# Performance work log

Measured on AMD Instinct MI355X. Metric: run time of the kernel, lower is better.

Reference implementation:

```python
import jax, jax.numpy as jnp
import numpy as np

N = 100000        # nodes
E = 3200000       # edges (avg degree 32)
B = 64            # graphs in the batch
IN_DIM = 128
HEADS = 4
C1 = 8            # conv1 out_channels per head
C2 = 4            # conv2 out_channels per head
OUT_DIM = 10
EPS = 1e-16       # PyG softmax denominator eps


def _lin(key, fan_in, fan_out):
    return jax.random.normal(key, (fan_in, fan_out), jnp.float32) / np.sqrt(fan_in)


def setup_inputs() -> dict:
    key = jax.random.key(0)
    ks = jax.random.split(key, 16)
    x = jax.random.normal(ks[0], (N, IN_DIM), jnp.float32)
    edge_index = jax.random.randint(ks[1], (2, E), 0, N)
    batch = jnp.sort(jax.random.randint(ks[2], (N,), 0, B))
    d1 = HEADS * C1  # 32
    d2 = HEADS * C2  # 16
    inp = {
        "x": x, "edge_index": edge_index, "batch": batch,
        # conv1 (TransformerConv in=128 -> heads*8 = 32)
        "Wq1": _lin(ks[3], IN_DIM, d1), "bq1": jnp.zeros((d1,), jnp.float32),
        "Wk1": _lin(ks[4], IN_DIM, d1), "bk1": jnp.zeros((d1,), jnp.float32),
        "Wv1": _lin(ks[5], IN_DIM, d1), "bv1": jnp.zeros((d1,), jnp.float32),
        "Ws1": _lin(ks[6], IN_DIM, d1), "bs1": jnp.zeros((d1,), jnp.float32),
        # conv2 (in=32 -> heads*4 = 16)
        "Wq2": _lin(ks[7], d1, d2), "bq2": jnp.zeros((d2,), jnp.float32),
        "Wk2": _lin(ks[8], d1, d2), "bk2": jnp.zeros((d2,), jnp.float32),
        "Wv2": _lin(ks[9], d1, d2), "bv2": jnp.zeros((d2,), jnp.float32),
        "Ws2": _lin(ks[10], d1, d2), "bs2": jnp.zeros((d2,), jnp.float32),
        # fc (16 -> 10)
        "Wfc": _lin(ks[11], d2, OUT_DIM), "bfc": jnp.zeros((OUT_DIM,), jnp.float32),
    }
    return inp


def transformer_conv(x, src, dst, Wq, bq, Wk, bk, Wv, bv, Ws, bs, heads):
    n = x.shape[0]
    hc = Wq.shape[1]
    c = hc // heads
    q = (x @ Wq + bq).reshape(n, heads, c)
    k = (x @ Wk + bk).reshape(n, heads, c)
    v = (x @ Wv + bv).reshape(n, heads, c)
    # edge-wise attention logits: query at dst, key at src -> [E, H]
    alpha = jnp.einsum('ehc,ehc->eh', q[dst], k[src]) / np.sqrt(c).astype(np.float32)
    # segment softmax over incoming edges of each dst node
    amax = jax.ops.segment_max(alpha, dst, num_segments=n)           # [N,H]
    ea = jnp.exp(alpha - amax[dst])
    denom = jax.ops.segment_sum(ea, dst, num_segments=n)             # [N,H]
    w = ea / (denom[dst] + EPS)                                      # [E,H]
    msg = v[src] * w[:, :, None]                                     # [E,H,C]
    out = jax.ops.segment_sum(msg, dst, num_segments=n).reshape(n, hc)
    return out + x @ Ws + bs  # root/skip connection


def reference(x, edge_index, batch,
              Wq1, bq1, Wk1, bk1, Wv1, bv1, Ws1, bs1,
              Wq2, bq2, Wk2, bk2, Wv2, bv2, Ws2, bs2,
              Wfc, bfc):
    src, dst = edge_index[0], edge_index[1]
    h = transformer_conv(x, src, dst, Wq1, bq1, Wk1, bk1, Wv1, bv1, Ws1, bs1, HEADS)
    h = jax.nn.relu(h)
    h = transformer_conv(h, src, dst, Wq2, bq2, Wk2, bk2, Wv2, bv2, Ws2, bs2, HEADS)
    h = jax.nn.relu(h)
    # global mean pool per graph
    sums = jax.ops.segment_sum(h, batch, num_segments=B)             # [B,16]
    cnt = jax.ops.segment_sum(jnp.ones((h.shape[0],), h.dtype), batch, num_segments=B)
    pooled = sums / jnp.maximum(cnt, 1.0)[:, None]
    return pooled @ Wfc + bfc                                        # [B,OUT_DIM]
```

## Files before the change

kernel.cpp:

```cpp
#include <hip/hip_runtime.h>

#define HEADS 4
#define EPS 1e-16f
#define NR 256
#define EPB 2048

typedef float floatx2 __attribute__((ext_vector_type(2)));
typedef short bf16x8 __attribute__((ext_vector_type(8)));
typedef float f32x4 __attribute__((ext_vector_type(4)));

__device__ inline unsigned short f2bf(float f) {
    union { float f; unsigned u; } v; v.f = f;
    unsigned r = v.u + 0x7FFFu + ((v.u >> 16) & 1u);
    return (unsigned short)(r >> 16);
}
__device__ inline unsigned char f2fp8(float f) {
    return (unsigned char)(__builtin_amdgcn_cvt_pk_fp8_f32(f, 0.f, 0u, false) & 0xFF);
}

__device__ inline int rangeOf(int dst, int rdiv, float rinv) {
    int q = (int)((float)dst * rinv);
    if (q > NR - 1) q = NR - 1;
    if ((long long)q * rdiv > dst) --q;
    else if ((long long)(q + 1) * rdiv <= dst) ++q;
    return q;
}

__global__ __launch_bounds__(256) void scatter_count(
    const int* __restrict__ ei, int E, int rdiv, float rinv,
    int* __restrict__ pcnt)
{
    __shared__ int cnt[NR];
    int b = blockIdx.x, t = threadIdx.x;
    int b0 = b * EPB;
    int nloc = min(EPB, E - b0);
    cnt[t] = 0;
    __syncthreads();
    #pragma unroll
    for (int u = 0; u < 8; ++u) {
        int li = u * 256 + t;
        if (li < nloc)
            atomicAdd(&cnt[rangeOf(ei[E + b0 + li], rdiv, rinv)], 1);
    }
    __syncthreads();
    pcnt[(size_t)b * NR + t] = cnt[t];
}

__global__ __launch_bounds__(256) void qprefix(
    int* __restrict__ pcnt, int nb, int* __restrict__ qtot)
{
    __shared__ int part[256];
    int q = blockIdx.x, t = threadIdx.x;
    int per = (nb + 255) >> 8;
    int lo = t * per, hi = min(lo + per, nb);
    int s = 0;
    for (int b = lo; b < hi; ++b) s += pcnt[(size_t)b * NR + q];
    part[t] = s;
    __syncthreads();
    for (int off = 1; off < 256; off <<= 1) {
        int a = (t >= off) ? part[t - off] : 0;
        __syncthreads();
        part[t] += a;
        __syncthreads();
    }
    if (t == 255) qtot[q] = part[255];
    int pre = (t == 0) ? 0 : part[t - 1];
    for (int b = lo; b < hi; ++b) {
        int c = pcnt[(size_t)b * NR + q];
        pcnt[(size_t)b * NR + q] = pre;
        pre += c;
    }
}

__global__ void qscan(const int* __restrict__ qtot, int* __restrict__ rstart)
{
    __shared__ int tmp[NR];
    int t = threadIdx.x;
    tmp[t] = qtot[t];
    __syncthreads();
    for (int off = 1; off < NR; off <<= 1) {
        int a = (t >= off) ? tmp[t - off] : 0;
        __syncthreads();
        tmp[t] += a;
        __syncthreads();
    }
    rstart[t] = (t == 0) ? 0 : tmp[t - 1];
    if (t == NR - 1) rstart[NR] = tmp[NR - 1];
}

__global__ __launch_bounds__(256) void scatter_place(
    const int* __restrict__ ei, int E, int rdiv, float rinv,
    const int* __restrict__ pcnt, const int* __restrict__ rstart,
    int* __restrict__ rsrc, int* __restrict__ rdst)
{
    __shared__ int2 lrec[EPB];
    __shared__ unsigned char lq[EPB];
    __shared__ int cnt[NR], base[NR], scn[NR];
    int b = blockIdx.x, t = threadIdx.x;
    int b0 = b * EPB;
    int nloc = min(EPB, E - b0);
    cnt[t] = 0;
    __syncthreads();
    int myq[8], myoff[8];
    int2 myrec[8];
    #pragma unroll
    for (int u = 0; u < 8; ++u) {
        int li = u * 256 + t;
        if (li < nloc) {
            int e = b0 + li;
            int sv = ei[e], dv = ei[E + e];
            int q = rangeOf(dv, rdiv, rinv);
            myq[u] = q;
            myrec[u] = make_int2(sv, dv);
            myoff[u] = atomicAdd(&cnt[q], 1);
        } else myq[u] = -1;
    }
    __syncthreads();
    scn[t] = cnt[t];
    __syncthreads();
    for (int off = 1; off < 256; off <<= 1) {
        int a = (t >= off) ? scn[t - off] : 0;
        __syncthreads();
        scn[t] += a;
        __syncthreads();
    }
    base[t] = (t == 0) ? 0 : scn[t - 1];
    __syncthreads();
    #pragma unroll
    for (int u = 0; u < 8; ++u) {
        if (myq[u] >= 0) {
            int slot = base[myq[u]] + myoff[u];
            lrec[slot] = myrec[u];
            lq[slot] = (unsigned char)myq[u];
        }
    }
    __syncthreads();
    #pragma unroll
    for (int u = 0; u < 8; ++u) {
        int s2 = u * 256 + t;
        if (s2 < nloc) {
            int q = lq[s2];
            int g = rstart[q] + pcnt[(size_t)b * NR + q] + (s2 - base[q]);
            int2 r = lrec[s2];
            rsrc[g] = r.x;
            rdst[g] = r.y;
        }
    }
}

__global__ __launch_bounds__(256) void deg_range(
    const int* __restrict__ rdst, const int* __restrict__ rstart,
    int* __restrict__ deg, int* __restrict__ row_ptr,
    int* __restrict__ phd, int n, int rdiv, int E)
{
    __shared__ int h[512];
    __shared__ int psum[256];
    __shared__ int hd[256];
    int q = blockIdx.x, t = threadIdx.x;
    int lo = q * rdiv, hi = min(lo + rdiv, n);
    int nn = hi - lo;
    if (nn <= 0) {
        phd[q * 256 + t] = 0;
        if (t == 0 && q == NR - 1) row_ptr[n] = E;
        return;
    }
    h[t] = 0; h[t + 256] = 0; hd[t] = 0;
    __syncthreads();
    int rlo = rstart[q], rhi = rstart[q + 1];
    for (int i = rlo + t; i < rhi; i += 256)
        atomicAdd(&h[rdst[i] - lo], 1);
    __syncthreads();
    int s0 = h[2 * t], s1 = h[2 * t + 1];
    psum[t] = s0 + s1;
    __syncthreads();
    for (int off = 1; off < 256; off <<= 1) {
        int a = (t >= off) ? psum[t - off] : 0;
        __syncthreads();
        psum[t] += a;
        __syncthreads();
    }
    int base = rlo + ((t == 0) ? 0 : psum[t - 1]);
    if (2 * t < nn) {
        row_ptr[lo + 2 * t] = base;
        deg[lo + 2 * t] = s0;
        atomicAdd(&hd[min(s0, 255)], 1);
    }
    if (2 * t + 1 < nn) {
        row_ptr[lo + 2 * t + 1] = base + s0;
        deg[lo + 2 * t + 1] = s1;
        atomicAdd(&hd[min(s1, 255)], 1);
    }
    if (t == 0 && q == NR - 1) row_ptr[n] = E;
    __syncthreads();
    phd[q * 256 + t] = hd[t];
}

__global__ __launch_bounds__(256) void dsort_scanA(
    int* __restrict__ phd, int* __restrict__ tot)
{
    __shared__ int tmp[256];
    int bin = blockIdx.x, t = threadIdx.x;
    int v = phd[t * 256 + bin];
    tmp[t] = v;
    __syncthreads();
    for (int off = 1; off < 256; off <<= 1) {
        int a = (t >= off) ? tmp[t - off] : 0;
        __syncthreads();
        tmp[t] += a;
        __syncthreads();
    }
    phd[t * 256 + bin] = tmp[t] - v;
    if (t == 255) tot[bin] = tmp[255];
}

__global__ void dsort_scanB(int* __restrict__ tot)
{
    __shared__ int tmp[256];
    int t = threadIdx.x;
    int v = tot[t];
    tmp[t] = v;
    __syncthreads();
    for (int off = 1; off < 256; off <<= 1) {
        int a = (t >= off) ? tmp[t - off] : 0;
        __syncthreads();
        tmp[t] += a;
        __syncthreads();
    }
    tot[t] = tmp[t] - v;
}

__global__ __launch_bounds__(256) void dsort_addC(
    int* __restrict__ phd, const int* __restrict__ tot)
{
    int t = threadIdx.x;
    phd[blockIdx.x * 256 + t] += tot[t];
}

__global__ __launch_bounds__(256) void place_range(
    const int* __restrict__ rsrc, const int* __restrict__ rdst,
    const int* __restrict__ rstart, const int* __restrict__ row_ptr,
    const int* __restrict__ deg, const int* __restrict__ phd,
    int* __restrict__ col, int* __restrict__ order, int n, int rdiv)
{
    __shared__ int cur[512];
    __shared__ int lcur[256];
    int q = blockIdx.x, t = threadIdx.x;
    int lo = q * rdiv, hi = min(lo + rdiv, n);
    int nn = hi - lo;
    if (nn <= 0) return;
    for (int i = t; i < nn; i += 256) cur[i] = row_ptr[lo + i];
    lcur[t] = phd[q * 256 + t];
    __syncthreads();
    int rlo = rstart[q], rhi = rstart[q + 1];
    for (int i = rlo + t; i < rhi; i += 256) {
        int pos = atomicAdd(&cur[rdst[i] - lo], 1);
        col[pos] = rsrc[i];
    }
    for (int i = t; i < nn; i += 256) {
        int pos = atomicAdd(&lcur[min(deg[lo + i], 255)], 1);
        order[pos] = lo + i;
    }
}

__global__ __launch_bounds__(256) void pack_w1(
    const float* __restrict__ Wq, const float* __restrict__ Wk,
    const float* __restrict__ Wv, const float* __restrict__ Ws,
    unsigned short* __restrict__ wp)
{
    int tid = blockIdx.x * 256 + threadIdx.x;
    int s = tid >> 9, c = (tid >> 6) & 7, l = tid & 63;
    int gcol = c * 16 + (l & 15);
    int sub = gcol >> 5, j = gcol & 31;
    const float* W = (sub == 0) ? Wq : (sub == 1) ? Wk : (sub == 2) ? Wv : Ws;
    int k0 = s * 32 + ((l >> 4) << 3);
    unsigned short v[8];
    #pragma unroll
    for (int jj = 0; jj < 8; ++jj) v[jj] = f2bf(W[(size_t)(k0 + jj) * 32 + j]);
    uint4 o;
    o.x = v[0] | ((unsigned)v[1] << 16);
    o.y = v[2] | ((unsigned)v[3] << 16);
    o.z = v[4] | ((unsigned)v[5] << 16);
    o.w = v[6] | ((unsigned)v[7] << 16);
    *(uint4*)(wp + (size_t)tid * 8) = o;
}

__global__ void pack_w2(
    const float* __restrict__ Wq, const float* __restrict__ Wk,
    const float* __restrict__ Wv, const float* __restrict__ Ws,
    unsigned short* __restrict__ wp)
{
    int tid = threadIdx.x;
    int c = tid >> 6, l = tid & 63;
    int gcol = c * 16 + (l & 15);
    int sub = gcol >> 4, j = gcol & 15;
    const float* W = (sub == 0) ? Wq : (sub == 1) ? Wk : (sub == 2) ? Wv : Ws;
    int k0 = (l >> 4) << 3;
    unsigned short v[8];
    #pragma unroll
    for (int jj = 0; jj < 8; ++jj) v[jj] = f2bf(W[(size_t)(k0 + jj) * 16 + j]);
    uint4 o;
    o.x = v[0] | ((unsigned)v[1] << 16);
    o.y = v[2] | ((unsigned)v[3] << 16);
    o.z = v[4] | ((unsigned)v[5] << 16);
    o.w = v[6] | ((unsigned)v[7] << 16);
    *(uint4*)(wp + (size_t)tid * 8) = o;
}

__global__ __launch_bounds__(256) void proj1_mfma(
    const float* __restrict__ x, const unsigned short* __restrict__ wp,
    const float* __restrict__ bq, const float* __restrict__ bk,
    const float* __restrict__ bv, const float* __restrict__ bs,
    float* __restrict__ qs1, unsigned char* __restrict__ kv1, int n)
{
    int w = threadIdx.x >> 6, l = threadIdx.x & 63;
    int row0 = blockIdx.x * 64 + w * 16;
    if (row0 >= n) return;
    int arow = row0 + (l & 15);
    f32x4 c0 = {0,0,0,0}, c1 = {0,0,0,0}, c2 = {0,0,0,0}, c3 = {0,0,0,0};
    f32x4 c4 = {0,0,0,0}, c5 = {0,0,0,0}, c6 = {0,0,0,0}, c7 = {0,0,0,0};
    const uint4* wp4 = (const uint4*)wp;
    #pragma unroll
    for (int s = 0; s < 4; ++s) {
        union { uint4 u; bf16x8 b; } av;
        if (arow < n) {
            const float* xp = x + (size_t)arow * 128 + s * 32 + ((l >> 4) << 3);
            float4 x0 = *(const float4*)xp;
            float4 x1 = *(const float4*)(xp + 4);
            av.u.x = f2bf(x0.x) | ((unsigned)f2bf(x0.y) << 16);
            av.u.y = f2bf(x0.z) | ((unsigned)f2bf(x0.w) << 16);
            av.u.z = f2bf(x1.x) | ((unsigned)f2bf(x1.y) << 16);
            av.u.w = f2bf(x1.z) | ((unsigned)f2bf(x1.w) << 16);
        } else {
            av.u = make_uint4(0, 0, 0, 0);
        }
        const uint4* base = wp4 + (size_t)(s * 8) * 64 + l;
        union { uint4 u; bf16x8 b; } bc;
        bc.u = base[0 * 64]; c0 = __builtin_amdgcn_mfma_f32_16x16x32_bf16(av.b, bc.b, c0, 0, 0, 0);
        bc.u = base[1 * 64]; c1 = __builtin_amdgcn_mfma_f32_16x16x32_bf16(av.b, bc.b, c1, 0, 0, 0);
        bc.u = base[2 * 64]; c2 = __builtin_amdgcn_mfma_f32_16x16x32_bf16(av.b, bc.b, c2, 0, 0, 0);
        bc.u = base[3 * 64]; c3 = __builtin_amdgcn_mfma_f32_16x16x32_bf16(av.b, bc.b, c3, 0, 0, 0);
        bc.u = base[4 * 64]; c4 = __builtin_amdgcn_mfma_f32_16x16x32_bf16(av.b, bc.b, c4, 0, 0, 0);
        bc.u = base[5 * 64]; c5 = __builtin_amdgcn_mfma_f32_16x16x32_bf16(av.b, bc.b, c5, 0, 0, 0);
        bc.u = base[6 * 64]; c6 = __builtin_amdgcn_mfma_f32_16x16x32_bf16(av.b, bc.b, c6, 0, 0, 0);
        bc.u = base[7 * 64]; c7 = __builtin_amdgcn_mfma_f32_16x16x32_bf16(av.b, bc.b, c7, 0, 0, 0);
    }
    int rbase = row0 + ((l >> 4) << 2);
    int lc = l & 15;
    float bq0 = bq[lc], bq1 = bq[16 + lc];
    float bk0 = bk[lc], bk1 = bk[16 + lc];
    float bv0 = bv[lc], bv1 = bv[16 + lc];
    float bs0 = bs[lc], bs1 = bs[16 + lc];
    #pragma unroll
    for (int r = 0; r < 4; ++r) {
        int row = rbase + r;
        if (row < n) {
            float* q = qs1 + (size_t)row * 64;
            unsigned char* kvp = kv1 + (size_t)row * 64;
            q[lc]      = c0[r] + bq0;
            q[16 + lc] = c1[r] + bq1;
            q[32 + lc] = c6[r] + bs0;
            q[48 + lc] = c7[r] + bs1;
            kvp[lc]      = f2fp8(c2[r] + bk0);
            kvp[16 + lc] = f2fp8(c3[r] + bk1);
            kvp[32 + lc] = f2fp8(c4[r] + bv0);
            kvp[48 + lc] = f2fp8(c5[r] + bv1);
        }
    }
}

__global__ __launch_bounds__(256) void proj2_mfma(
    const float* __restrict__ h1, const unsigned short* __restrict__ wp,
    const float* __restrict__ bq, const float* __restrict__ bk,
    const float* __restrict__ bv, const float* __restrict__ bs,
    float* __restrict__ qs2, unsigned char* __restrict__ kv2, int n)
{
    int w = threadIdx.x >> 6, l = threadIdx.x & 63;
    int row0 = blockIdx.x * 64 + w * 16;
    if (row0 >= n) return;
    int arow = row0 + (l & 15);
    f32x4 c0 = {0,0,0,0}, c1 = {0,0,0,0}, c2 = {0,0,0,0}, c3 = {0,0,0,0};
    union { uint4 u; bf16x8 b; } av;
    if (arow < n) {
        const float* xp = h1 + (size_t)arow * 32 + ((l >> 4) << 3);
        float4 x0 = *(const float4*)xp;
        float4 x1 = *(const float4*)(xp + 4);
        av.u.x = f2bf(x0.x) | ((unsigned)f2bf(x0.y) << 16);
        av.u.y = f2bf(x0.z) | ((unsigned)f2bf(x0.w) << 16);
        av.u.z = f2bf(x1.x) | ((unsigned)f2bf(x1.y) << 16);
        av.u.w = f2bf(x1.z) | ((unsigned)f2bf(x1.w) << 16);
    } else {
        av.u = make_uint4(0, 0, 0, 0);
    }
    const uint4* base = (const uint4*)wp + l;
    union { uint4 u; bf16x8 b; } bc;
    bc.u = base[0];   c0 = __builtin_amdgcn_mfma_f32_16x16x32_bf16(av.b, bc.b, c0, 0, 0, 0);
    bc.u = base[64];  c1 = __builtin_amdgcn_mfma_f32_16x16x32_bf16(av.b, bc.b, c1, 0, 0, 0);
    bc.u = base[128]; c2 = __builtin_amdgcn_mfma_f32_16x16x32_bf16(av.b, bc.b, c2, 0, 0, 0);
    bc.u = base[192]; c3 = __builtin_amdgcn_mfma_f32_16x16x32_bf16(av.b, bc.b, c3, 0, 0, 0);
    int rbase = row0 + ((l >> 4) << 2);
    int lc = l & 15;
    float bq0 = bq[lc], bk0 = bk[lc], bv0 = bv[lc], bs0 = bs[lc];
    #pragma unroll
    for (int r = 0; r < 4; ++r) {
        int row = rbase + r;
        if (row < n) {
            float* q = qs2 + (size_t)row * 32;
            unsigned char* kvp = kv2 + (size_t)row * 32;
            q[lc]        = c0[r] + bq0;
            q[16 + lc]   = c3[r] + bs0;
            kvp[lc]      = f2fp8(c1[r] + bk0);
            kvp[16 + lc] = f2fp8(c2[r] + bv0);
        }
    }
}

__global__ __launch_bounds__(256) void gather_conv1(
    const int* __restrict__ row_ptr, const int* __restrict__ order,
    const int* __restrict__ col, const float* __restrict__ qs1,
    const unsigned char* __restrict__ kv1, float* __restrict__ h1, int n)
{
    int tid = blockIdx.x * 256 + threadIdx.x;
    if (tid >= n * HEADS) return;
    int node = order[tid >> 2], h = tid & 3;
    const float4* qp = (const float4*)(qs1 + (size_t)node * 64 + h * 8);
    float4 q0 = qp[0], q1 = qp[1];
    int start = row_ptr[node], d = row_ptr[node + 1] - start;
    float m = -INFINITY, s = 0.f;
    float a0x=0,a0y=0,a0z=0,a0w=0,a1x=0,a1y=0,a1z=0,a1w=0;
    uint2 ku = make_uint2(0,0), vu = make_uint2(0,0);
    if (d > 0) {
        const unsigned char* b0 = kv1 + (size_t)col[start] * 64;
        ku = *(const uint2*)(b0 + h * 8);
        vu = *(const uint2*)(b0 + 32 + h * 8);
    }
    for (int i = 0; i < d; ++i) {
        uint2 kn = ku, vn = vu;
        if (i + 1 < d) {
            const unsigned char* nb = kv1 + (size_t)col[start + i + 1] * 64;
            kn = *(const uint2*)(nb + h * 8);
            vn = *(const uint2*)(nb + 32 + h * 8);
        }
        floatx2 k01 = __builtin_amdgcn_cvt_pk_f32_fp8(ku.x, false);
        floatx2 k23 = __builtin_amdgcn_cvt_pk_f32_fp8(ku.x, true);
        floatx2 k45 = __builtin_amdgcn_cvt_pk_f32_fp8(ku.y, false);
        floatx2 k67 = __builtin_amdgcn_cvt_pk_f32_fp8(ku.y, true);
        float a = (q0.x*k01.x + q0.y*k01.y + q0.z*k23.x + q0.w*k23.y
                 + q1.x*k45.x + q1.y*k45.y + q1.z*k67.x + q1.w*k67.y)
                * 0.35355339059327373f;
        float mn = fmaxf(m, a);
        float corr = __expf(m - mn);
        float ea = __expf(a - mn);
        s = s * corr + ea;
        floatx2 v01 = __builtin_amdgcn_cvt_pk_f32_fp8(vu.x, false);
        floatx2 v23 = __builtin_amdgcn_cvt_pk_f32_fp8(vu.x, true);
        floatx2 v45 = __builtin_amdgcn_cvt_pk_f32_fp8(vu.y, false);
        floatx2 v67 = __builtin_amdgcn_cvt_pk_f32_fp8(vu.y, true);
        a0x = a0x*corr + ea*v01.x; a0y = a0y*corr + ea*v01.y;
        a0z = a0z*corr + ea*v23.x; a0w = a0w*corr + ea*v23.y;
        a1x = a1x*corr + ea*v45.x; a1y = a1y*corr + ea*v45.y;
        a1z = a1z*corr + ea*v67.x; a1w = a1w*corr + ea*v67.y;
        m = mn;
        ku = kn; vu = vn;
    }
    float inv = 1.f / (s + EPS);
    const float* sk = qs1 + (size_t)node * 64 + 32 + h * 8;
    float4 o0, o1;
    o0.x = fmaxf(a0x*inv + sk[0], 0.f); o0.y = fmaxf(a0y*inv + sk[1], 0.f);
    o0.z = fmaxf(a0z*inv + sk[2], 0.f); o0.w = fmaxf(a0w*inv + sk[3], 0.f);
    o1.x = fmaxf(a1x*inv + sk[4], 0.f); o1.y = fmaxf(a1y*inv + sk[5], 0.f);
    o1.z = fmaxf(a1z*inv + sk[6], 0.f); o1.w = fmaxf(a1w*inv + sk[7], 0.f);
    float4* op = (float4*)(h1 + (size_t)node * 32 + h * 8);
    op[0] = o0; op[1] = o1;
}

__global__ __launch_bounds__(256) void gather_conv2(
    const int* __restrict__ row_ptr, const int* __restrict__ order,
    const int* __restrict__ col, const float* __restrict__ qs2,
    const unsigned char* __restrict__ kv2, float* __restrict__ h2, int n)
{
    int tid = blockIdx.x * 256 + threadIdx.x;
    if (tid >= n * HEADS) return;
    int node = order[tid >> 2], h = tid & 3;
    float4 q = *(const float4*)(qs2 + (size_t)node * 32 + h * 4);
    int start = row_ptr[node], d = row_ptr[node + 1] - start;
    float m = -INFINITY, s = 0.f;
    float ax=0, ay=0, az=0, aw=0;
    unsigned ku = 0, vu = 0;
    if (d > 0) {
        const unsigned char* b0 = kv2 + (size_t)col[start] * 32;
        ku = *(const unsigned*)(b0 + h * 4);
        vu = *(const unsigned*)(b0 + 16 + h * 4);
    }
    for (int i = 0; i < d; ++i) {
        unsigned kn = ku, vn = vu;
        if (i + 1 < d) {
            const unsigned char* nb = kv2 + (size_t)col[start + i + 1] * 32;
            kn = *(const unsigned*)(nb + h * 4);
            vn = *(const unsigned*)(nb + 16 + h * 4);
        }
        floatx2 k01 = __builtin_amdgcn_cvt_pk_f32_fp8(ku, false);
        floatx2 k23 = __builtin_amdgcn_cvt_pk_f32_fp8(ku, true);
        float a = (q.x*k01.x + q.y*k01.y + q.z*k23.x + q.w*k23.y) * 0.5f;
        float mn = fmaxf(m, a);
        float corr = __expf(m - mn);
        float ea = __expf(a - mn);
        s = s * corr + ea;
        floatx2 v01 = __builtin_amdgcn_cvt_pk_f32_fp8(vu, false);
        floatx2 v23 = __builtin_amdgcn_cvt_pk_f32_fp8(vu, true);
        ax = ax*corr + ea*v01.x; ay = ay*corr + ea*v01.y;
        az = az*corr + ea*v23.x; aw = aw*corr + ea*v23.y;
        m = mn;
        ku = kn; vu = vn;
    }
    float inv = 1.f / (s + EPS);
    const float* sk = qs2 + (size_t)node * 32 + 16 + h * 4;
    float4 o;
    o.x = fmaxf(ax*inv + sk[0], 0.f);
    o.y = fmaxf(ay*inv + sk[1], 0.f);
    o.z = fmaxf(az*inv + sk[2], 0.f);
    o.w = fmaxf(aw*inv + sk[3], 0.f);
    *(float4*)(h2 + (size_t)node * 16 + h * 4) = o;
}

__global__ __launch_bounds__(256) void pool_kernel(
    const float* __restrict__ h2, const int* __restrict__ batch,
    float* __restrict__ pooled, float* __restrict__ cnt, int n)
{
    __shared__ float acc[16];
    __shared__ int bShared;
    __shared__ int uniform;
    int node0 = blockIdx.x * 16;
    int t = threadIdx.x;
    int node = node0 + (t >> 4), j = t & 15;
    if (t == 0) {
        int bFirst = batch[node0];
        int bLast = batch[min(node0 + 15, n - 1)];
        bShared = bFirst;
        uniform = (bFirst == bLast);
    }
    if (t < 16) acc[t] = 0.f;
    __syncthreads();
    bool active = node < n;
    float val = active ? h2[(size_t)node * 16 + j] : 0.f;
    if (uniform) {
        if (active) atomicAdd(&acc[j], val);
        __syncthreads();
        int nlocal = min(16, n - node0);
        if (t < 16) atomicAdd(pooled + bShared * 16 + t, acc[t]);
        if (t == 0) atomicAdd(cnt + bShared, (float)nlocal);
    } else {
        if (active) {
            int b = batch[node];
            atomicAdd(pooled + b * 16 + j, val);
            if (j == 0) atomicAdd(cnt + b, 1.f);
        }
    }
}

__global__ void fc_kernel(
    const float* __restrict__ pooled, const float* __restrict__ cnt,
    const float* __restrict__ Wfc, const float* __restrict__ bfc,
    float* __restrict__ out)
{
    int t = threadIdx.x;
    if (t < 64 * 10) {
        int b = t / 10, o = t % 10;
        float c = fmaxf(cnt[b], 1.0f);
        float acc = bfc[o];
        #pragma unroll
        for (int k = 0; k < 16; ++k)
            acc += (pooled[b * 16 + k] / c) * Wfc[k * 10 + o];
        out[t] = acc;
    }
}

extern "C" void kernel_launch(void* const* d_in, const int* in_sizes, int n_in,
                              void* d_out, int out_size, void* d_ws, size_t ws_size,
                              hipStream_t stream) {
    const float* x     = (const float*)d_in[0];
    const int*   ei    = (const int*)d_in[1];
    const int*   batch = (const int*)d_in[2];
    const float* Wq1 = (const float*)d_in[3],  *bq1 = (const float*)d_in[4];
    const float* Wk1 = (const float*)d_in[5],  *bk1 = (const float*)d_in[6];
    const float* Wv1 = (const float*)d_in[7],  *bv1 = (const float*)d_in[8];
    const float* Ws1 = (const float*)d_in[9],  *bs1 = (const float*)d_in[10];
    const float* Wq2 = (const float*)d_in[11], *bq2 = (const float*)d_in[12];
    const float* Wk2 = (const float*)d_in[13], *bk2 = (const float*)d_in[14];
    const float* Wv2 = (const float*)d_in[15], *bv2 = (const float*)d_in[16];
    const float* Ws2 = (const float*)d_in[17], *bs2 = (const float*)d_in[18];
    const float* Wfc = (const float*)d_in[19], *bfc = (const float*)d_in[20];

    int N = in_sizes[0] / 128;
    int E = in_sizes[1] / 2;
    int rdiv = (N + NR - 1) / NR;
    float rinv = 1.0f / (float)rdiv;
    int NB = (E + EPB - 1) / EPB;

    float* ws = (float*)d_ws;
    float* qs1    = ws;
    float* h1     = qs1 + (size_t)N * 64;
    float* h2     = h1 + (size_t)N * 32;
    float* qs2    = h2 + (size_t)N * 16;
    float* pooled = qs2 + (size_t)N * 32;
    float* cnt    = pooled + 1024;
    unsigned char* kv1 = (unsigned char*)(cnt + 64);
    unsigned char* kv2 = kv1 + (size_t)N * 64;
    int* deg     = (int*)(kv2 + (size_t)N * 32);
    int* row_ptr = deg + N;
    int* rstart  = row_ptr + N + 1;
    int* qtot    = rstart + NR + 1;
    int* col     = qtot + NR;
    int* order   = col + E;
    int* pcnt    = order + N;
    int* phd     = pcnt + (size_t)NB * NR;
    unsigned short* wp1 = (unsigned short*)(phd + (size_t)NR * 256);
    unsigned short* wp2 = wp1 + 16384;
    int* rsrc = (int*)h1;
    int* rdst = (int*)h2;

    hipMemsetAsync(pooled, 0, (1024 + 64) * sizeof(float), stream);

    int ngrid = (N * HEADS + 255) / 256;
    int mtiles = (N + 63) / 64;

    pack_w1<<<8, 256, 0, stream>>>(Wq1, Wk1, Wv1, Ws1, wp1);
    pack_w2<<<1, 256, 0, stream>>>(Wq2, Wk2, Wv2, Ws2, wp2);

    scatter_count<<<NB, 256, 0, stream>>>(ei, E, rdiv, rinv, pcnt);
    qprefix<<<NR, 256, 0, stream>>>(pcnt, NB, qtot);
    qscan<<<1, NR, 0, stream>>>(qtot, rstart);
    scatter_place<<<NB, 256, 0, stream>>>(ei, E, rdiv, rinv, pcnt, rstart, rsrc, rdst);
    deg_range<<<NR, 256, 0, stream>>>(rdst, rstart, deg, row_ptr, phd, N, rdiv, E);
    dsort_scanA<<<NR, 256, 0, stream>>>(phd, qtot);
    dsort_scanB<<<1, 256, 0, stream>>>(qtot);
    dsort_addC<<<NR, 256, 0, stream>>>(phd, qtot);
    place_range<<<NR, 256, 0, stream>>>(rsrc, rdst, rstart, row_ptr, deg, phd, col, order, N, rdiv);

    proj1_mfma<<<mtiles, 256, 0, stream>>>(x, wp1, bq1, bk1, bv1, bs1, qs1, kv1, N);
    gather_conv1<<<ngrid, 256, 0, stream>>>(row_ptr, order, col, qs1, kv1, h1, N);

    proj2_mfma<<<mtiles, 256, 0, stream>>>(h1, wp2, bq2, bk2, bv2, bs2, qs2, kv2, N);
    gather_conv2<<<ngrid, 256, 0, stream>>>(row_ptr, order, col, qs2, kv2, h2, N);

    pool_kernel<<<(N + 15) / 16, 256, 0, stream>>>(h2, batch, pooled, cnt, N);
    fc_kernel<<<1, 640, 0, stream>>>(pooled, cnt, Wfc, bfc, (float*)d_out);
}
```

Measured before the change: 318.7 us.

## Fuse CSR column placement into degree kernel and deepen gather index prefetch

The column-placement scatter moves into the degree/row_ptr kernel, which reuses its in-shared-memory prefix sums as cursors and drops a second pass over the range-partitioned edges. The degree-sort add step is folded into a new order-placement kernel, so the chain launches one fewer kernel. Both gather kernels now load the column index two edges ahead and the key/value row one edge ahead, which hides the dependent index-then-data load latency. The cost is extra shared memory and a longer serial tail in the degree kernel, plus clamped redundant index loads at the end of each row.

```diff
diff --git a/kernel.cpp b/kernel.cpp
--- a/kernel.cpp
+++ b/kernel.cpp
@@ -148,12 +148,14 @@
     }
 }
 
-__global__ __launch_bounds__(256) void deg_range(
-    const int* __restrict__ rdst, const int* __restrict__ rstart,
-    int* __restrict__ deg, int* __restrict__ row_ptr,
-    int* __restrict__ phd, int n, int rdiv, int E)
+__global__ __launch_bounds__(256) void deg_range_place(
+    const int* __restrict__ rsrc, const int* __restrict__ rdst,
+    const int* __restrict__ rstart,
+    int* __restrict__ deg, int* __restrict__ row_ptr, int* __restrict__ phd,
+    int* __restrict__ col, int n, int rdiv, int E)
 {
     __shared__ int h[512];
+    __shared__ int cur[512];
     __shared__ int psum[256];
     __shared__ int hd[256];
     int q = blockIdx.x, t = threadIdx.x;
@@ -180,6 +182,8 @@
         __syncthreads();
     }
     int base = rlo + ((t == 0) ? 0 : psum[t - 1]);
+    cur[2 * t] = base;
+    cur[2 * t + 1] = base + s0;
     if (2 * t < nn) {
         row_ptr[lo + 2 * t] = base;
         deg[lo + 2 * t] = s0;
@@ -193,6 +197,10 @@
     if (t == 0 && q == NR - 1) row_ptr[n] = E;
     __syncthreads();
     phd[q * 256 + t] = hd[t];
+    for (int i = rlo + t; i < rhi; i += 256) {
+        int pos = atomicAdd(&cur[rdst[i] - lo], 1);
+        col[pos] = rsrc[i];
+    }
 }
 
 __global__ __launch_bounds__(256) void dsort_scanA(
@@ -229,36 +237,18 @@
     tot[t] = tmp[t] - v;
 }
 
-__global__ __launch_bounds__(256) void dsort_addC(
-    int* __restrict__ phd, const int* __restrict__ tot)
-{
-    int t = threadIdx.x;
-    phd[blockIdx.x * 256 + t] += tot[t];
-}
-
-__global__ __launch_bounds__(256) void place_range(
-    const int* __restrict__ rsrc, const int* __restrict__ rdst,
-    const int* __restrict__ rstart, const int* __restrict__ row_ptr,
-    const int* __restrict__ deg, const int* __restrict__ phd,
-    int* __restrict__ col, int* __restrict__ order, int n, int rdiv)
-{
-    __shared__ int cur[512];
+__global__ __launch_bounds__(256) void dsort_place(
+    const int* __restrict__ phd, const int* __restrict__ tot,
+    const int* __restrict__ deg, int* __restrict__ order, int n, int rdiv)
+{
     __shared__ int lcur[256];
     int q = blockIdx.x, t = threadIdx.x;
+    lcur[t] = phd[q * 256 + t] + tot[t];
+    __syncthreads();
     int lo = q * rdiv, hi = min(lo + rdiv, n);
-    int nn = hi - lo;
-    if (nn <= 0) return;
-    for (int i = t; i < nn; i += 256) cur[i] = row_ptr[lo + i];
-    lcur[t] = phd[q * 256 + t];
-    __syncthreads();
-    int rlo = rstart[q], rhi = rstart[q + 1];
-    for (int i = rlo + t; i < rhi; i += 256) {
-        int pos = atomicAdd(&cur[rdst[i] - lo], 1);
-        col[pos] = rsrc[i];
-    }
-    for (int i = t; i < nn; i += 256) {
-        int pos = atomicAdd(&lcur[min(deg[lo + i], 255)], 1);
-        order[pos] = lo + i;
+    for (int i = lo + t; i < hi; i += 256) {
+        int pos = atomicAdd(&lcur[min(deg[i], 255)], 1);
+        order[pos] = i;
     }
 }
 
@@ -427,40 +417,39 @@
     int start = row_ptr[node], d = row_ptr[node + 1] - start;
     float m = -INFINITY, s = 0.f;
     float a0x=0,a0y=0,a0z=0,a0w=0,a1x=0,a1y=0,a1z=0,a1w=0;
-    uint2 ku = make_uint2(0,0), vu = make_uint2(0,0);
     if (d > 0) {
+        int dm1 = d - 1;
         const unsigned char* b0 = kv1 + (size_t)col[start] * 64;
-        ku = *(const uint2*)(b0 + h * 8);
-        vu = *(const uint2*)(b0 + 32 + h * 8);
-    }
-    for (int i = 0; i < d; ++i) {
-        uint2 kn = ku, vn = vu;
-        if (i + 1 < d) {
-            const unsigned char* nb = kv1 + (size_t)col[start + i + 1] * 64;
-            kn = *(const uint2*)(nb + h * 8);
-            vn = *(const uint2*)(nb + 32 + h * 8);
-        }
-        floatx2 k01 = __builtin_amdgcn_cvt_pk_f32_fp8(ku.x, false);
-        floatx2 k23 = __builtin_amdgcn_cvt_pk_f32_fp8(ku.x, true);
-        floatx2 k45 = __builtin_amdgcn_cvt_pk_f32_fp8(ku.y, false);
-        floatx2 k67 = __builtin_amdgcn_cvt_pk_f32_fp8(ku.y, true);
-        float a = (q0.x*k01.x + q0.y*k01.y + q0.z*k23.x + q0.w*k23.y
-                 + q1.x*k45.x + q1.y*k45.y + q1.z*k67.x + q1.w*k67.y)
-                * 0.35355339059327373f;
-        float mn = fmaxf(m, a);
-        float corr = __expf(m - mn);
-        float ea = __expf(a - mn);
-        s = s * corr + ea;
-        floatx2 v01 = __builtin_amdgcn_cvt_pk_f32_fp8(vu.x, false);
-        floatx2 v23 = __builtin_amdgcn_cvt_pk_f32_fp8(vu.x, true);
-        floatx2 v45 = __builtin_amdgcn_cvt_pk_f32_fp8(vu.y, false);
-        floatx2 v67 = __builtin_amdgcn_cvt_pk_f32_fp8(vu.y, true);
-        a0x = a0x*corr + ea*v01.x; a0y = a0y*corr + ea*v01.y;
-        a0z = a0z*corr + ea*v23.x; a0w = a0w*corr + ea*v23.y;
-        a1x = a1x*corr + ea*v45.x; a1y = a1y*corr + ea*v45.y;
-        a1z = a1z*corr + ea*v67.x; a1w = a1w*corr + ea*v67.y;
-        m = mn;
-        ku = kn; vu = vn;
+        uint2 ku = *(const uint2*)(b0 + h * 8);
+        uint2 vu = *(const uint2*)(b0 + 32 + h * 8);
+        int c1 = col[start + min(1, dm1)];
+        for (int i = 0; i < d; ++i) {
+            int c2 = col[start + min(i + 2, dm1)];
+            const unsigned char* nb = kv1 + (size_t)c1 * 64;
+            uint2 kn = *(const uint2*)(nb + h * 8);
+            uint2 vn = *(const uint2*)(nb + 32 + h * 8);
+            floatx2 k01 = __builtin_amdgcn_cvt_pk_f32_fp8(ku.x, false);
+            floatx2 k23 = __builtin_amdgcn_cvt_pk_f32_fp8(ku.x, true);
+            floatx2 k45 = __builtin_amdgcn_cvt_pk_f32_fp8(ku.y, false);
+            floatx2 k67 = __builtin_amdgcn_cvt_pk_f32_fp8(ku.y, true);
+            float a = (q0.x*k01.x + q0.y*k01.y + q0.z*k23.x + q0.w*k23.y
+                     + q1.x*k45.x + q1.y*k45.y + q1.z*k67.x + q1.w*k67.y)
+                    * 0.35355339059327373f;
+            float mn = fmaxf(m, a);
+            float corr = __expf(m - mn);
+            float ea = __expf(a - mn);
+            s = s * corr + ea;
+            floatx2 v01 = __builtin_amdgcn_cvt_pk_f32_fp8(vu.x, false);
+            floatx2 v23 = __builtin_amdgcn_cvt_pk_f32_fp8(vu.x, true);
+            floatx2 v45 = __builtin_amdgcn_cvt_pk_f32_fp8(vu.y, false);
+            floatx2 v67 = __builtin_amdgcn_cvt_pk_f32_fp8(vu.y, true);
+            a0x = a0x*corr + ea*v01.x; a0y = a0y*corr + ea*v01.y;
+            a0z = a0z*corr + ea*v23.x; a0w = a0w*corr + ea*v23.y;
+            a1x = a1x*corr + ea*v45.x; a1y = a1y*corr + ea*v45.y;
+            a1z = a1z*corr + ea*v67.x; a1w = a1w*corr + ea*v67.y;
+            m = mn;
+            ku = kn; vu = vn; c1 = c2;
+        }
     }
     float inv = 1.f / (s + EPS);
     const float* sk = qs1 + (size_t)node * 64 + 32 + h * 8;
@@ -485,32 +474,31 @@
     int start = row_ptr[node], d = row_ptr[node + 1] - start;
     float m = -INFINITY, s = 0.f;
     float ax=0, ay=0, az=0, aw=0;
-    unsigned ku = 0, vu = 0;
     if (d > 0) {
+        int dm1 = d - 1;
         const unsigned char* b0 = kv2 + (size_t)col[start] * 32;
-        ku = *(const unsigned*)(b0 + h * 4);
-        vu = *(const unsigned*)(b0 + 16 + h * 4);
-    }
-    for (int i = 0; i < d; ++i) {
-        unsigned kn = ku, vn = vu;
-        if (i + 1 < d) {
-            const unsigned char* nb = kv2 + (size_t)col[start + i + 1] * 32;
-            kn = *(const unsigned*)(nb + h * 4);
-            vn = *(const unsigned*)(nb + 16 + h * 4);
-        }
-        floatx2 k01 = __builtin_amdgcn_cvt_pk_f32_fp8(ku, false);
-        floatx2 k23 = __builtin_amdgcn_cvt_pk_f32_fp8(ku, true);
-        float a = (q.x*k01.x + q.y*k01.y + q.z*k23.x + q.w*k23.y) * 0.5f;
-        float mn = fmaxf(m, a);
-        float corr = __expf(m - mn);
-        float ea = __expf(a - mn);
-        s = s * corr + ea;
-        floatx2 v01 = __builtin_amdgcn_cvt_pk_f32_fp8(vu, false);
-        floatx2 v23 = __builtin_amdgcn_cvt_pk_f32_fp8(vu, true);
-        ax = ax*corr + ea*v01.x; ay = ay*corr + ea*v01.y;
-        az = az*corr + ea*v23.x; aw = aw*corr + ea*v23.y;
-        m = mn;
-        ku = kn; vu = vn;
+        unsigned ku = *(const unsigned*)(b0 + h * 4);
+        unsigned vu = *(const unsigned*)(b0 + 16 + h * 4);
+        int c1 = col[start + min(1, dm1)];
+        for (int i = 0; i < d; ++i) {
+            int c2 = col[start + min(i + 2, dm1)];
+            const unsigned char* nb = kv2 + (size_t)c1 * 32;
+            unsigned kn = *(const unsigned*)(nb + h * 4);
+            unsigned vn = *(const unsigned*)(nb + 16 + h * 4);
+            floatx2 k01 = __builtin_amdgcn_cvt_pk_f32_fp8(ku, false);
+            floatx2 k23 = __builtin_amdgcn_cvt_pk_f32_fp8(ku, true);
+            float a = (q.x*k01.x + q.y*k01.y + q.z*k23.x + q.w*k23.y) * 0.5f;
+            float mn = fmaxf(m, a);
+            float corr = __expf(m - mn);
+            float ea = __expf(a - mn);
+            s = s * corr + ea;
+            floatx2 v01 = __builtin_amdgcn_cvt_pk_f32_fp8(vu, false);
+            floatx2 v23 = __builtin_amdgcn_cvt_pk_f32_fp8(vu, true);
+            ax = ax*corr + ea*v01.x; ay = ay*corr + ea*v01.y;
+            az = az*corr + ea*v23.x; aw = aw*corr + ea*v23.y;
+            m = mn;
+            ku = kn; vu = vn; c1 = c2;
+        }
     }
     float inv = 1.f / (s + EPS);
     const float* sk = qs2 + (size_t)node * 32 + 16 + h * 4;
@@ -630,11 +618,10 @@
     qprefix<<<NR, 256, 0, stream>>>(pcnt, NB, qtot);
     qscan<<<1, NR, 0, stream>>>(qtot, rstart);
     scatter_place<<<NB, 256, 0, stream>>>(ei, E, rdiv, rinv, pcnt, rstart, rsrc, rdst);
-    deg_range<<<NR, 256, 0, stream>>>(rdst, rstart, deg, row_ptr, phd, N, rdiv, E);
+    deg_range_place<<<NR, 256, 0, stream>>>(rsrc, rdst, rstart, deg, row_ptr, phd, col, N, rdiv, E);
     dsort_scanA<<<NR, 256, 0, stream>>>(phd, qtot);
     dsort_scanB<<<1, 256, 0, stream>>>(qtot);
-    dsort_addC<<<NR, 256, 0, stream>>>(phd, qtot);
-    place_range<<<NR, 256, 0, stream>>>(rsrc, rdst, rstart, row_ptr, deg, phd, col, order, N, rdiv);
+    dsort_place<<<NR, 256, 0, stream>>>(phd, qtot, deg, order, N, rdiv);
 
     proj1_mfma<<<mtiles, 256, 0, stream>>>(x, wp1, bq1, bk1, bv1, bs1, qs1, kv1, N);
     gather_conv1<<<ngrid, 256, 0, stream>>>(row_ptr, order, col, qs1, kv1, h1, N);
```

Measured after the change: 314.3 us. About the same (-1.4%).
